# Kernel tuning notes

Hardware: AMD Instinct MI355X
Metric: run time of the kernel (lower is better)

The kernel has to match this reference:

```python
import jax, jax.numpy as jnp
import numpy as np

N = 50000      # nodes
E = 800000     # edges
F_IN = 128     # in_channels
H = 128        # hidden_channels
C = 10         # num_classes
G = 512        # graphs in batch
EPS = 1e-5     # batchnorm eps


def setup_inputs() -> dict:
    key = jax.random.key(0)
    ks = jax.random.split(key, 18)
    s = 0.05
    return {
        "x": jax.random.normal(ks[0], (N, F_IN), jnp.float32),
        "edge_index": jax.random.randint(ks[1], (2, E), 0, N, dtype=jnp.int32),
        "batch": jnp.sort(jax.random.randint(ks[2], (N,), 0, G, dtype=jnp.int32)),
        "W1": jax.random.normal(ks[3], (F_IN, H), jnp.float32) * s,
        "b1": jnp.zeros((H,), jnp.float32),
        "gamma1": jnp.ones((H,), jnp.float32),
        "beta1": jnp.zeros((H,), jnp.float32),
        "mean1": jax.random.normal(ks[4], (H,), jnp.float32) * 0.1,
        "var1": jax.random.uniform(ks[5], (H,), jnp.float32, 0.5, 1.5),
        "W2": jax.random.normal(ks[6], (H, H), jnp.float32) * s,
        "b2": jnp.zeros((H,), jnp.float32),
        "gamma2": jnp.ones((H,), jnp.float32),
        "beta2": jnp.zeros((H,), jnp.float32),
        "mean2": jax.random.normal(ks[7], (H,), jnp.float32) * 0.1,
        "var2": jax.random.uniform(ks[8], (H,), jnp.float32, 0.5, 1.5),
        "Wlin": jax.random.normal(ks[9], (H, C), jnp.float32) * s,
        "blin": jnp.zeros((C,), jnp.float32),
    }


def _gcn_conv(x, W, b, src, dst):
    # GCNConv with add_self_loops=True, symmetric normalization.
    h = x @ W                                             # [N, H]
    deg = jax.ops.segment_sum(jnp.ones((E,), h.dtype), dst, num_segments=N) + 1.0
    dis = jax.lax.rsqrt(deg)                              # deg^{-1/2}, [N]
    norm = dis[src] * dis[dst]                            # [E]
    agg = jax.ops.segment_sum(h[src] * norm[:, None], dst, num_segments=N)
    agg = agg + h * (dis * dis)[:, None]                  # self-loop term
    return agg + b


def _bn_eval(x, gamma, beta, mean, var):
    return gamma * (x - mean) * jax.lax.rsqrt(var + EPS) + beta


def reference(x, edge_index, batch, W1, b1, gamma1, beta1, mean1, var1,
              W2, b2, gamma2, beta2, mean2, var2, Wlin, blin):
    src, dst = edge_index[0], edge_index[1]
    h = _gcn_conv(x, W1, b1, src, dst)
    h = jax.nn.relu(_bn_eval(h, gamma1, beta1, mean1, var1))
    # dropout: identity in eval mode
    h = _gcn_conv(h, W2, b2, src, dst)
    h = jax.nn.relu(_bn_eval(h, gamma2, beta2, mean2, var2))
    # global_mean_pool over graph ids
    sums = jax.ops.segment_sum(h, batch, num_segments=G)          # [G, H]
    cnts = jax.ops.segment_sum(jnp.ones((N,), h.dtype), batch, num_segments=G)
    pooled = sums / jnp.maximum(cnts, 1.0)[:, None]
    return pooled @ Wlin + blin                                   # [G, C]
```

## Files before the change

### kernel.cpp

```cpp
#include <hip/hip_runtime.h>
#include <hip/hip_bf16.h>

#define N_NODES 50000
#define N_EDGES 800000
#define HDIM 128
#define NGRAPH 512
#define NCLS 10
#define BN_EPS 1e-5f
#define MAXDEG 64

typedef unsigned int  uint32;
typedef unsigned short ushort16;

__device__ inline float2 bf2f(uint32 u) {
    return make_float2(__uint_as_float(u << 16), __uint_as_float(u & 0xffff0000u));
}
__device__ inline ushort16 f2bf(float f) {
    uint32 u = __float_as_uint(f);
    u += 0x7fffu + ((u >> 16) & 1u);
    return (ushort16)(u >> 16);
}
__device__ inline uint32 packbf2(float lo, float hi) {
    return (uint32)f2bf(lo) | ((uint32)f2bf(hi) << 16);
}

__global__ __launch_bounds__(256) void bucket_edges(const int* __restrict__ src,
                                                    const int* __restrict__ dst,
                                                    int* __restrict__ deg,
                                                    int* __restrict__ epad, int ne)
{
    int e = blockIdx.x * 256 + threadIdx.x;
    if (e >= ne) return;
    int d   = dst[e];
    int pos = atomicAdd(&deg[d], 1);
    epad[(size_t)d * MAXDEG + pos] = src[e];
}

__global__ __launch_bounds__(256) void rsqrt_deg(const int* __restrict__ deg,
                                                 float* __restrict__ dis, int n)
{
    int i = blockIdx.x * 256 + threadIdx.x;
    if (i < n) dis[i] = rsqrtf((float)deg[i] + 1.0f);
}

template <typename TIN>
__global__ __launch_bounds__(256) void gemm_nk128(const TIN* __restrict__ X,
                                                  const float* __restrict__ W,
                                                  ushort16* __restrict__ Y, int nrows)
{
    __shared__ float xs[32][36];
    __shared__ float ws[32][128];
    const int t    = threadIdx.x;
    const int row0 = blockIdx.x * 32;
    const int tx   = t & 31;
    const int ty   = t >> 5;

    float acc[4][4];
    #pragma unroll
    for (int i = 0; i < 4; ++i)
        #pragma unroll
        for (int j = 0; j < 4; ++j) acc[i][j] = 0.f;

    const int lr = t >> 3;
    const int lk = (t & 7) << 2;
    const int wr = t >> 5;
    const int wc = (t & 31) << 2;

    for (int k0 = 0; k0 < 128; k0 += 32) {
        float4 xv = make_float4(0.f, 0.f, 0.f, 0.f);
        int grow = row0 + lr;
        if (grow < nrows) {
            const TIN* p = X + (size_t)grow * HDIM + k0 + lk;
            if constexpr (sizeof(TIN) == 4) {
                xv = *(const float4*)p;
            } else {
                uint2 u = *(const uint2*)p;
                float2 a = bf2f(u.x), bb = bf2f(u.y);
                xv = make_float4(a.x, a.y, bb.x, bb.y);
            }
        }
        xs[lr][lk] = xv.x; xs[lr][lk + 1] = xv.y; xs[lr][lk + 2] = xv.z; xs[lr][lk + 3] = xv.w;
        #pragma unroll
        for (int i = 0; i < 4; ++i) {
            int kk = wr + i * 8;
            *(float4*)&ws[kk][wc] = *(const float4*)(W + (size_t)(k0 + kk) * HDIM + wc);
        }
        __syncthreads();
        #pragma unroll
        for (int kk = 0; kk < 32; kk += 4) {
            float4 wv[4];
            #pragma unroll
            for (int j = 0; j < 4; ++j) wv[j] = *(const float4*)&ws[kk + j][tx << 2];
            #pragma unroll
            for (int i = 0; i < 4; ++i) {
                float4 xr = *(const float4*)&xs[ty * 4 + i][kk];
                acc[i][0] += xr.x * wv[0].x; acc[i][1] += xr.x * wv[0].y;
                acc[i][2] += xr.x * wv[0].z; acc[i][3] += xr.x * wv[0].w;
                acc[i][0] += xr.y * wv[1].x; acc[i][1] += xr.y * wv[1].y;
                acc[i][2] += xr.y * wv[1].z; acc[i][3] += xr.y * wv[1].w;
                acc[i][0] += xr.z * wv[2].x; acc[i][1] += xr.z * wv[2].y;
                acc[i][2] += xr.z * wv[2].z; acc[i][3] += xr.z * wv[2].w;
                acc[i][0] += xr.w * wv[3].x; acc[i][1] += xr.w * wv[3].y;
                acc[i][2] += xr.w * wv[3].z; acc[i][3] += xr.w * wv[3].w;
            }
        }
        __syncthreads();
    }
    #pragma unroll
    for (int i = 0; i < 4; ++i) {
        int grow = row0 + ty * 4 + i;
        if (grow < nrows) {
            uint2 o;
            o.x = packbf2(acc[i][0], acc[i][1]);
            o.y = packbf2(acc[i][2], acc[i][3]);
            *(uint2*)(Y + (size_t)grow * HDIM + (tx << 2)) = o;
        }
    }
}

__global__ __launch_bounds__(256) void gather_bn_relu(const ushort16* __restrict__ h,
                                                      const int* __restrict__ epad,
                                                      const int* __restrict__ deg,
                                                      const float* __restrict__ dis,
                                                      const float* __restrict__ b,
                                                      const float* __restrict__ gamma,
                                                      const float* __restrict__ beta,
                                                      const float* __restrict__ mean,
                                                      const float* __restrict__ var,
                                                      ushort16* __restrict__ out, int n)
{
    int node = blockIdx.x * 4 + (threadIdx.x >> 6);
    if (node >= n) return;
    const int lane = threadIdx.x & 63;
    const int q    = lane >> 4;
    const int ci   = (lane & 15) << 3;
    const int cnt_e = deg[node];
    const int base  = node * MAXDEG;
    const float dd  = dis[node];

    int   s_all  = 0;
    float nm_all = 0.f;
    if (lane < cnt_e) {
        s_all  = epad[base + lane];
        nm_all = dis[s_all] * dd;
    }

    float acc[8] = {0.f, 0.f, 0.f, 0.f, 0.f, 0.f, 0.f, 0.f};
    for (int j = q; j < cnt_e; j += 4) {
        int   s  = __shfl(s_all, j);
        float nm = __shfl(nm_all, j);
        uint4 v  = *(const uint4*)(h + (size_t)s * HDIM + ci);
        float2 f0 = bf2f(v.x), f1 = bf2f(v.y), f2 = bf2f(v.z), f3 = bf2f(v.w);
        acc[0] += f0.x * nm; acc[1] += f0.y * nm;
        acc[2] += f1.x * nm; acc[3] += f1.y * nm;
        acc[4] += f2.x * nm; acc[5] += f2.y * nm;
        acc[6] += f3.x * nm; acc[7] += f3.y * nm;
    }
    #pragma unroll
    for (int k = 0; k < 8; ++k) {
        acc[k] += __shfl_xor(acc[k], 16);
        acc[k] += __shfl_xor(acc[k], 32);
    }

    if (q == 0) {
        uint4 hv = *(const uint4*)(h + (size_t)node * HDIM + ci);
        float2 g0 = bf2f(hv.x), g1 = bf2f(hv.y), g2 = bf2f(hv.z), g3 = bf2f(hv.w);
        float dd2 = dd * dd;
        float a[8] = {acc[0] + g0.x * dd2, acc[1] + g0.y * dd2,
                      acc[2] + g1.x * dd2, acc[3] + g1.y * dd2,
                      acc[4] + g2.x * dd2, acc[5] + g2.y * dd2,
                      acc[6] + g3.x * dd2, acc[7] + g3.y * dd2};
        float o[8];
        #pragma unroll
        for (int k = 0; k < 8; ++k) {
            int c = ci + k;
            float sc = gamma[c] * rsqrtf(var[c] + BN_EPS);
            float r  = (a[k] + b[c] - mean[c]) * sc + beta[c];
            o[k] = fmaxf(r, 0.f);
        }
        uint4 ov;
        ov.x = packbf2(o[0], o[1]); ov.y = packbf2(o[2], o[3]);
        ov.z = packbf2(o[4], o[5]); ov.w = packbf2(o[6], o[7]);
        *(uint4*)(out + (size_t)node * HDIM + ci) = ov;
    }
}

__global__ __launch_bounds__(128) void pool_sum(const ushort16* __restrict__ h,
                                                const int* __restrict__ batch,
                                                float* __restrict__ sums,
                                                float* __restrict__ cnt, int n)
{
    int c  = threadIdx.x;
    int n0 = blockIdx.x * 32;
    if (n0 >= n) return;
    int nend = min(n0 + 32, n);
    int curg = batch[n0];
    float acc = 0.f;
    int run = 0;
    for (int i = n0; i < nend; ++i) {
        int g   = batch[i];
        float v = __uint_as_float((uint32)h[(size_t)i * HDIM + c] << 16);
        if (g != curg) {
            atomicAdd(&sums[(size_t)curg * HDIM + c], acc);
            if (c == 0) atomicAdd(&cnt[curg], (float)run);
            acc = 0.f; run = 0; curg = g;
        }
        acc += v; run++;
    }
    atomicAdd(&sums[(size_t)curg * HDIM + c], acc);
    if (c == 0) atomicAdd(&cnt[curg], (float)run);
}

__global__ __launch_bounds__(128) void final_lin(const float* __restrict__ sums,
                                                 const float* __restrict__ cnt,
                                                 const float* __restrict__ Wlin,
                                                 const float* __restrict__ blin,
                                                 float* __restrict__ out)
{
    __shared__ float red[NCLS][2];
    int g = blockIdx.x;
    int t = threadIdx.x;
    float ic = 1.f / fmaxf(cnt[g], 1.f);
    float v  = sums[(size_t)g * HDIM + t] * ic;
    float p[NCLS];
    #pragma unroll
    for (int c = 0; c < NCLS; ++c) p[c] = v * Wlin[t * NCLS + c];
    #pragma unroll
    for (int c = 0; c < NCLS; ++c) {
        float x = p[c];
        for (int off = 32; off > 0; off >>= 1) x += __shfl_down(x, off);
        if ((t & 63) == 0) red[c][t >> 6] = x;
    }
    __syncthreads();
    if (t < NCLS) out[g * NCLS + t] = red[t][0] + red[t][1] + blin[t];
}

extern "C" void kernel_launch(void* const* d_in, const int* in_sizes, int n_in,
                              void* d_out, int out_size, void* d_ws, size_t ws_size,
                              hipStream_t stream)
{
    const float* x     = (const float*)d_in[0];
    const int*   ei    = (const int*)d_in[1];
    const int*   srcp  = ei;
    const int*   dstp  = ei + N_EDGES;
    const int*   batch = (const int*)d_in[2];
    const float* W1    = (const float*)d_in[3];
    const float* b1    = (const float*)d_in[4];
    const float* g1    = (const float*)d_in[5];
    const float* be1   = (const float*)d_in[6];
    const float* m1    = (const float*)d_in[7];
    const float* v1    = (const float*)d_in[8];
    const float* W2    = (const float*)d_in[9];
    const float* b2    = (const float*)d_in[10];
    const float* g2    = (const float*)d_in[11];
    const float* be2   = (const float*)d_in[12];
    const float* m2    = (const float*)d_in[13];
    const float* v2    = (const float*)d_in[14];
    const float* Wlin  = (const float*)d_in[15];
    const float* blin  = (const float*)d_in[16];
    float*       out   = (float*)d_out;

    ushort16* bufA = (ushort16*)d_ws;
    ushort16* bufB = bufA + (size_t)N_NODES * HDIM;
    int*   epad = (int*)(bufB + (size_t)N_NODES * HDIM);
    int*   deg  = epad + (size_t)N_NODES * MAXDEG;
    float* cnt  = (float*)(deg + N_NODES);
    float* sums = cnt + NGRAPH;
    float* dis  = sums + (size_t)NGRAPH * HDIM;

    hipMemsetAsync(deg, 0,
                   (N_NODES + NGRAPH + (size_t)NGRAPH * HDIM) * sizeof(float), stream);

    bucket_edges<<<(N_EDGES + 255) / 256, 256, 0, stream>>>(srcp, dstp, deg, epad, N_EDGES);
    rsqrt_deg<<<(N_NODES + 255) / 256, 256, 0, stream>>>(deg, dis, N_NODES);

    const int gemm_blocks   = (N_NODES + 31) / 32;
    const int gather_blocks = (N_NODES + 3) / 4;

    gemm_nk128<float><<<gemm_blocks, 256, 0, stream>>>(x, W1, bufA, N_NODES);
    gather_bn_relu<<<gather_blocks, 256, 0, stream>>>(bufA, epad, deg, dis,
                                                      b1, g1, be1, m1, v1, bufB, N_NODES);
    gemm_nk128<ushort16><<<gemm_blocks, 256, 0, stream>>>(bufB, W2, bufA, N_NODES);
    gather_bn_relu<<<gather_blocks, 256, 0, stream>>>(bufA, epad, deg, dis,
                                                      b2, g2, be2, m2, v2, bufB, N_NODES);
    pool_sum<<<(N_NODES + 31) / 32, 128, 0, stream>>>(bufB, batch, sums, cnt, N_NODES);
    final_lin<<<NGRAPH, 128, 0, stream>>>(sums, cnt, Wlin, blin, out);
}
```

Baseline: 300.7 us.

## Merge edge bucketing and first GEMM into one interleaved front kernel

Result: faster. 279.7 us (-7.0%).

```diff
diff --git a/kernel.cpp b/kernel.cpp
--- a/kernel.cpp
+++ b/kernel.cpp
@@ -24,36 +24,36 @@
     return (uint32)f2bf(lo) | ((uint32)f2bf(hi) << 16);
 }
 
-__global__ __launch_bounds__(256) void bucket_edges(const int* __restrict__ src,
-                                                    const int* __restrict__ dst,
-                                                    int* __restrict__ deg,
-                                                    int* __restrict__ epad, int ne)
-{
-    int e = blockIdx.x * 256 + threadIdx.x;
-    if (e >= ne) return;
-    int d   = dst[e];
-    int pos = atomicAdd(&deg[d], 1);
-    epad[(size_t)d * MAXDEG + pos] = src[e];
-}
-
-__global__ __launch_bounds__(256) void rsqrt_deg(const int* __restrict__ deg,
-                                                 float* __restrict__ dis, int n)
-{
-    int i = blockIdx.x * 256 + threadIdx.x;
-    if (i < n) dis[i] = rsqrtf((float)deg[i] + 1.0f);
-}
-
-template <typename TIN>
-__global__ __launch_bounds__(256) void gemm_nk128(const TIN* __restrict__ X,
-                                                  const float* __restrict__ W,
-                                                  ushort16* __restrict__ Y, int nrows)
+
+#define GEMM1_BLOCKS 1563
+#define FRONT_GRID (3 * GEMM1_BLOCKS)
+
+__global__ __launch_bounds__(256) void front(const float* __restrict__ x,
+                                             const float* __restrict__ W1,
+                                             ushort16* __restrict__ bufA,
+                                             const int* __restrict__ src,
+                                             const int* __restrict__ dst,
+                                             int* __restrict__ deg,
+                                             int* __restrict__ epad)
 {
     __shared__ float xs[32][36];
     __shared__ float ws[32][128];
-    const int t    = threadIdx.x;
-    const int row0 = blockIdx.x * 32;
-    const int tx   = t & 31;
-    const int ty   = t >> 5;
+    const int tid = threadIdx.x;
+    const int grp = blockIdx.x / 3, rem = blockIdx.x % 3;
+
+    if (rem != 0) {
+        int e = (grp * 2 + (rem - 1)) * 256 + tid;
+        if (e < N_EDGES) {
+            int d   = dst[e];
+            int pos = atomicAdd(&deg[d], 1);
+            epad[(size_t)d * MAXDEG + pos] = src[e];
+        }
+        return;
+    }
+
+    const int row0 = grp * 32;
+    const int tx   = tid & 31;
+    const int ty   = tid >> 5;
 
     float acc[4][4];
     #pragma unroll
@@ -61,29 +61,20 @@
         #pragma unroll
         for (int j = 0; j < 4; ++j) acc[i][j] = 0.f;
 
-    const int lr = t >> 3;
-    const int lk = (t & 7) << 2;
-    const int wr = t >> 5;
-    const int wc = (t & 31) << 2;
+    const int lr = tid >> 3;
+    const int lk = (tid & 7) << 2;
+    const int wr = tid >> 5;
+    const int wc = (tid & 31) << 2;
 
     for (int k0 = 0; k0 < 128; k0 += 32) {
         float4 xv = make_float4(0.f, 0.f, 0.f, 0.f);
         int grow = row0 + lr;
-        if (grow < nrows) {
-            const TIN* p = X + (size_t)grow * HDIM + k0 + lk;
-            if constexpr (sizeof(TIN) == 4) {
-                xv = *(const float4*)p;
-            } else {
-                uint2 u = *(const uint2*)p;
-                float2 a = bf2f(u.x), bb = bf2f(u.y);
-                xv = make_float4(a.x, a.y, bb.x, bb.y);
-            }
-        }
+        if (grow < N_NODES) xv = *(const float4*)(x + (size_t)grow * HDIM + k0 + lk);
         xs[lr][lk] = xv.x; xs[lr][lk + 1] = xv.y; xs[lr][lk + 2] = xv.z; xs[lr][lk + 3] = xv.w;
         #pragma unroll
         for (int i = 0; i < 4; ++i) {
             int kk = wr + i * 8;
-            *(float4*)&ws[kk][wc] = *(const float4*)(W + (size_t)(k0 + kk) * HDIM + wc);
+            *(float4*)&ws[kk][wc] = *(const float4*)(W1 + (size_t)(k0 + kk) * HDIM + wc);
         }
         __syncthreads();
         #pragma unroll
@@ -109,6 +100,82 @@
     #pragma unroll
     for (int i = 0; i < 4; ++i) {
         int grow = row0 + ty * 4 + i;
+        if (grow < N_NODES) {
+            uint2 o;
+            o.x = packbf2(acc[i][0], acc[i][1]);
+            o.y = packbf2(acc[i][2], acc[i][3]);
+            *(uint2*)(bufA + (size_t)grow * HDIM + (tx << 2)) = o;
+        }
+    }
+}
+
+__global__ __launch_bounds__(256) void rsqrt_deg(const int* __restrict__ deg_i,
+                                                 float* __restrict__ dis, int n)
+{
+    int i = blockIdx.x * 256 + threadIdx.x;
+    if (i < n) dis[i] = rsqrtf((float)deg_i[i] + 1.0f);
+}
+
+__global__ __launch_bounds__(256) void gemm2_nk128(const ushort16* __restrict__ X,
+                                                   const float* __restrict__ W,
+                                                   ushort16* __restrict__ Y, int nrows)
+{
+    __shared__ float xs[32][36];
+    __shared__ float ws[32][128];
+    const int t    = threadIdx.x;
+    const int row0 = blockIdx.x * 32;
+    const int tx   = t & 31;
+    const int ty   = t >> 5;
+
+    float acc[4][4];
+    #pragma unroll
+    for (int i = 0; i < 4; ++i)
+        #pragma unroll
+        for (int j = 0; j < 4; ++j) acc[i][j] = 0.f;
+
+    const int lr = t >> 3;
+    const int lk = (t & 7) << 2;
+    const int wr = t >> 5;
+    const int wc = (t & 31) << 2;
+
+    for (int k0 = 0; k0 < 128; k0 += 32) {
+        float4 xv = make_float4(0.f, 0.f, 0.f, 0.f);
+        int grow = row0 + lr;
+        if (grow < nrows) {
+            uint2 u = *(const uint2*)(X + (size_t)grow * HDIM + k0 + lk);
+            float2 a = bf2f(u.x), bb = bf2f(u.y);
+            xv = make_float4(a.x, a.y, bb.x, bb.y);
+        }
+        xs[lr][lk] = xv.x; xs[lr][lk + 1] = xv.y; xs[lr][lk + 2] = xv.z; xs[lr][lk + 3] = xv.w;
+        #pragma unroll
+        for (int i = 0; i < 4; ++i) {
+            int kk = wr + i * 8;
+            *(float4*)&ws[kk][wc] = *(const float4*)(W + (size_t)(k0 + kk) * HDIM + wc);
+        }
+        __syncthreads();
+        #pragma unroll
+        for (int kk = 0; kk < 32; kk += 4) {
+            float4 wv[4];
+            #pragma unroll
+            for (int j = 0; j < 4; ++j) wv[j] = *(const float4*)&ws[kk + j][tx << 2];
+            #pragma unroll
+            for (int i = 0; i < 4; ++i) {
+                float4 xr = *(const float4*)&xs[ty * 4 + i][kk];
+                acc[i][0] += xr.x * wv[0].x; acc[i][1] += xr.x * wv[0].y;
+                acc[i][2] += xr.x * wv[0].z; acc[i][3] += xr.x * wv[0].w;
+                acc[i][0] += xr.y * wv[1].x; acc[i][1] += xr.y * wv[1].y;
+                acc[i][2] += xr.y * wv[1].z; acc[i][3] += xr.y * wv[1].w;
+                acc[i][0] += xr.z * wv[2].x; acc[i][1] += xr.z * wv[2].y;
+                acc[i][2] += xr.z * wv[2].z; acc[i][3] += xr.z * wv[2].w;
+                acc[i][0] += xr.w * wv[3].x; acc[i][1] += xr.w * wv[3].y;
+                acc[i][2] += xr.w * wv[3].z; acc[i][3] += xr.w * wv[3].w;
+            }
+        }
+        __syncthreads();
+    }
+    #pragma unroll
+    for (int i = 0; i < 4; ++i) {
+        int grow = row0 + ty * 4 + i;
         if (grow < nrows) {
             uint2 o;
             o.x = packbf2(acc[i][0], acc[i][1]);
@@ -130,8 +197,8 @@
                                                       ushort16* __restrict__ out, int n)
 {
     int node = blockIdx.x * 4 + (threadIdx.x >> 6);
+    int lane = threadIdx.x & 63;
     if (node >= n) return;
-    const int lane = threadIdx.x & 63;
     const int q    = lane >> 4;
     const int ci   = (lane & 15) << 3;
     const int cnt_e = deg[node];
@@ -165,11 +232,10 @@
     if (q == 0) {
         uint4 hv = *(const uint4*)(h + (size_t)node * HDIM + ci);
         float2 g0 = bf2f(hv.x), g1 = bf2f(hv.y), g2 = bf2f(hv.z), g3 = bf2f(hv.w);
-        float dd2 = dd * dd;
-        float a[8] = {acc[0] + g0.x * dd2, acc[1] + g0.y * dd2,
-                      acc[2] + g1.x * dd2, acc[3] + g1.y * dd2,
-                      acc[4] + g2.x * dd2, acc[5] + g2.y * dd2,
-                      acc[6] + g3.x * dd2, acc[7] + g3.y * dd2};
+        float a[8] = {acc[0] + g0.x * dd * dd, acc[1] + g0.y * dd * dd,
+                      acc[2] + g1.x * dd * dd, acc[3] + g1.y * dd * dd,
+                      acc[4] + g2.x * dd * dd, acc[5] + g2.y * dd * dd,
+                      acc[6] + g3.x * dd * dd, acc[7] + g3.y * dd * dd};
         float o[8];
         #pragma unroll
         for (int k = 0; k < 8; ++k) {
@@ -271,16 +337,14 @@
     hipMemsetAsync(deg, 0,
                    (N_NODES + NGRAPH + (size_t)NGRAPH * HDIM) * sizeof(float), stream);
 
-    bucket_edges<<<(N_EDGES + 255) / 256, 256, 0, stream>>>(srcp, dstp, deg, epad, N_EDGES);
+    front<<<FRONT_GRID, 256, 0, stream>>>(x, W1, bufA, srcp, dstp, deg, epad);
     rsqrt_deg<<<(N_NODES + 255) / 256, 256, 0, stream>>>(deg, dis, N_NODES);
 
-    const int gemm_blocks   = (N_NODES + 31) / 32;
     const int gather_blocks = (N_NODES + 3) / 4;
 
-    gemm_nk128<float><<<gemm_blocks, 256, 0, stream>>>(x, W1, bufA, N_NODES);
     gather_bn_relu<<<gather_blocks, 256, 0, stream>>>(bufA, epad, deg, dis,
                                                       b1, g1, be1, m1, v1, bufB, N_NODES);
-    gemm_nk128<ushort16><<<gemm_blocks, 256, 0, stream>>>(bufB, W2, bufA, N_NODES);
+    gemm2_nk128<<<(N_NODES + 31) / 32, 256, 0, stream>>>(bufB, W2, bufA, N_NODES);
     gather_bn_relu<<<gather_blocks, 256, 0, stream>>>(bufA, epad, deg, dis,
                                                       b2, g2, be2, m2, v2, bufB, N_NODES);
     pool_sum<<<(N_NODES + 31) / 32, 128, 0, stream>>>(bufB, batch, sums, cnt, N_NODES);
```
